# Kernel optimization log

Hardware: AMD Instinct MI355X
Metric: run time of the kernel (lower is better)

The kernel has to match this reference:

```python
import jax, jax.numpy as jnp
import numpy as np
import math

B, S, E, H = 4, 1024, 1024, 16
D = E // H
C = 1.0           # Poincare ball curvature
CS = math.sqrt(C)
EPS = 1e-7

def _sq(x):
    return jnp.sum(x * x, axis=-1, keepdims=True)

def expmap0(v):
    n = jnp.sqrt(jnp.clip(_sq(v), 1e-15))
    return jnp.tanh(CS * n) * v / (CS * n)

def logmap0(y):
    n = jnp.sqrt(jnp.clip(_sq(y), 1e-15))
    t = jnp.clip(CS * n, 0.0, 1.0 - 1e-6)
    return jnp.arctanh(t) * y / (CS * n)

def hlinear(x, z, r):
    # Poincare fully-connected layer (HNN++, Shimizu et al.), as in hypll HLinear
    lam = 2.0 / jnp.clip(1.0 - C * _sq(x), EPS)          # [..., 1] conformal factor
    zn = jnp.clip(jnp.linalg.norm(z, axis=0), 1e-15)     # [out]
    xz = x @ z                                           # [..., out]
    tcr = 2.0 * CS * r
    v = (2.0 * zn / CS) * jnp.arcsinh(CS * lam * xz / zn * jnp.cosh(tcr) - (lam - 1.0) * jnp.sinh(tcr))
    w = jnp.sinh(CS * v) / CS
    return w / (1.0 + jnp.sqrt(1.0 + C * jnp.sum(w * w, -1, keepdims=True)))

def _beta(a, b):
    return math.exp(math.lgamma(a) + math.lgamma(b) - math.lgamma(a + b))

def _forward(query, key, value, zq, bq, zk, bk, zv, bv):
    pq, pk, pv = hlinear(query, zq, bq), hlinear(key, zk, bk), hlinear(value, zv, bv)
    split = lambda x: x.reshape(B, S, H, D).transpose(0, 2, 1, 3)   # [B,H,S,D]
    q, k, v = split(pq), split(pk), split(pv)
    # attention_similarity: negative per-head pairwise Poincare distance (all heads vectorized)
    q2 = jnp.sum(q * q, -1)                              # [B,H,Sq]
    k2 = jnp.sum(k * k, -1)                              # [B,H,Sk]
    qk = jnp.einsum('bhqd,bhkd->bhqk', q, k)
    diff2 = jnp.clip(q2[..., :, None] + k2[..., None, :] - 2.0 * qk, 0.0)
    den = jnp.clip((1.0 - C * q2)[..., :, None] * (1.0 - C * k2)[..., None, :], EPS)
    dist = jnp.arccosh(jnp.clip(1.0 + 2.0 * C * diff2 / den, 1.0 + 1e-6)) / CS
    # attention_activation: softmax over keys
    w = jax.nn.softmax(-dist, axis=-1)                   # [B,H,Sq,Sk]
    # attention_midpoint: weighted gyromidpoint of values over keys
    lam = 2.0 / jnp.clip(1.0 - C * jnp.sum(v * v, -1), EPS)          # [B,H,Sk]
    num = jnp.einsum('bhqk,bhkd->bhqd', w * lam[..., None, :], v)
    dnm = jnp.clip(jnp.einsum('bhqk,bhk->bhq', jnp.abs(w), lam - 1.0), EPS)
    u = num / dnm[..., None]
    mid = u / (1.0 + jnp.sqrt(jnp.clip(1.0 - C * _sq(u), EPS)))      # (1/2) Mobius scalar mult
    # manifold.cat: beta-concatenation of heads (HNN++)
    scale = _beta(E / 2.0, 0.5) / _beta(D / 2.0, 0.5)
    tv = logmap0(mid) * scale                            # tangent at origin, [B,H,S,D]
    return expmap0(tv.transpose(0, 2, 1, 3).reshape(B, S, E))

def setup_inputs():
    key = jax.random.key(0)
    ks = jax.random.split(key, 9)
    mk = lambda k: expmap0(jax.random.normal(k, (B, S, E), jnp.float32) * (0.3 / math.sqrt(E)))
    zs = lambda k: jax.random.normal(k, (E, E), jnp.float32) / math.sqrt(E)
    bs = lambda k: jax.random.normal(k, (E,), jnp.float32) * 0.01
    return {"query": mk(ks[0]), "key": mk(ks[1]), "value": mk(ks[2]),
            "zq": zs(ks[3]), "bq": bs(ks[4]), "zk": zs(ks[5]), "bk": bs(ks[6]),
            "zv": zs(ks[7]), "bv": bs(ks[8])}

def reference(query, key, value, zq, bq, zk, bk, zv, bv):
    return _forward(query, key, value, zq, bq, zk, bk, zv, bv)
```

## Files before the change

### kernel.cpp

```cpp
#include <hip/hip_runtime.h>
#include <cmath>

#define EPSF 1e-7f

constexpr int B_ = 4, S_ = 1024, E_ = 1024, H_ = 16, D_ = 64;
constexpr int BS_ = B_ * S_;

typedef __attribute__((ext_vector_type(8))) short bf16x8;
typedef __attribute__((ext_vector_type(4))) float f32x4;

__device__ inline unsigned int fbits(float f) { union { float f; unsigned int u; } x; x.f = f; return x.u; }
__device__ inline float ubits(unsigned int u) { union { unsigned int u; float f; } x; x.u = u; return x.f; }

__device__ inline unsigned short f2bf(float f) {
  unsigned int u = fbits(f);
  unsigned int r = u + 0x7fffu + ((u >> 16) & 1u);
  return (unsigned short)(r >> 16);
}
__device__ inline float bf2f(unsigned short h) { return ubits(((unsigned int)h) << 16); }
__device__ inline float fastrcp(float x) { return __builtin_amdgcn_rcpf(x); }
__device__ inline float fastsqrt(float x) { return __builtin_amdgcn_sqrtf(x); }

__device__ __forceinline__ void async_ld16(const unsigned short* g, unsigned short* l) {
  __builtin_amdgcn_global_load_lds(
      (const __attribute__((address_space(1))) unsigned int*)g,
      (__attribute__((address_space(3))) unsigned int*)l, 16, 0, 0);
}

__device__ __forceinline__ unsigned int cvt_pk_bf16(float lo, float hi) {
  unsigned int r;
  asm("v_cvt_pk_bf16_f32 %0, %1, %2" : "=v"(r) : "v"(lo), "v"(hi));
  return r;
}
__device__ __forceinline__ void permlane32_swap(unsigned int &a, unsigned int &b) {
  asm("v_permlane32_swap_b32 %0, %1" : "+v"(a), "+v"(b));
}
__device__ __forceinline__ void permlane16_swap(unsigned int &a, unsigned int &b) {
  asm("v_permlane16_swap_b32 %0, %1" : "+v"(a), "+v"(b));
}

__global__ __launch_bounds__(256) void prep_kernel(
    const float* __restrict__ xq, const float* __restrict__ xk,
    const float* __restrict__ xv, unsigned short* __restrict__ Xbf,
    float* __restrict__ lamRow,
    const float* __restrict__ zq, const float* __restrict__ zk, const float* __restrict__ zv,
    unsigned short* __restrict__ BhiT, float* __restrict__ Zpart) {
  const int bid = blockIdx.x;
  const int tid = threadIdx.x;
  if (bid < 3 * BS_ / 4) {
    const int wid = tid >> 6, lane = tid & 63;
    const int row = bid * 4 + wid;
    const float* x = (row < BS_) ? xq : (row < 2 * BS_ ? xk : xv);
    const int r = row & (BS_ - 1);
    const float4* src = (const float4*)(x + (size_t)r * E_);
    float4 v[4];
    #pragma unroll
    for (int j = 0; j < 4; j++) v[j] = src[lane + 64 * j];
    float s = 0.f;
    #pragma unroll
    for (int j = 0; j < 4; j++)
      s += v[j].x * v[j].x + v[j].y * v[j].y + v[j].z * v[j].z + v[j].w * v[j].w;
    #pragma unroll
    for (int m = 1; m < 64; m <<= 1) s += __shfl_xor(s, m, 64);
    uint2* dst = (uint2*)(Xbf + (size_t)row * E_);
    #pragma unroll
    for (int j = 0; j < 4; j++) {
      uint2 p;
      p.x = (unsigned int)f2bf(v[j].x) | ((unsigned int)f2bf(v[j].y) << 16);
      p.y = (unsigned int)f2bf(v[j].z) | ((unsigned int)f2bf(v[j].w) << 16);
      dst[lane + 64 * j] = p;
    }
    if (lane == 0) lamRow[row] = 2.0f / fmaxf(1.0f - s, EPSF);
    return;
  }
  const int lid = bid - 3 * BS_ / 4;
  const int mat = lid >> 8;
  const int rem = lid & 255;
  const int ky = rem >> 4, nx = rem & 15;
  const float* z = mat == 0 ? zq : (mat == 1 ? zk : zv);
  const int k0 = ky * 64, n0 = nx * 64;
  __shared__ float t[64][65];
  __shared__ float sred[64][4];
  {
    int kr = tid >> 4, nc = (tid & 15) * 4;
    #pragma unroll
    for (int i = 0; i < 4; i++) {
      float4 vv = *(const float4*)(z + (size_t)(k0 + kr + i * 16) * E_ + n0 + nc);
      t[kr + i * 16][nc + 0] = vv.x;
      t[kr + i * 16][nc + 1] = vv.y;
      t[kr + i * 16][nc + 2] = vv.z;
      t[kr + i * 16][nc + 3] = vv.w;
    }
  }
  __syncthreads();
  int nr = tid >> 2, kc = (tid & 3) * 16;
  unsigned int ph[8];
  float ss = 0.f;
  #pragma unroll
  for (int p = 0; p < 8; p++) {
    float x0 = t[kc + 2 * p][nr], x1 = t[kc + 2 * p + 1][nr];
    ph[p] = (unsigned int)f2bf(x0) | ((unsigned int)f2bf(x1) << 16);
    ss += x0 * x0 + x1 * x1;
  }
  size_t off = (size_t)mat * E_ * E_ + (size_t)(n0 + nr) * E_ + k0 + kc;
  uint4* dh = (uint4*)(BhiT + off);
  dh[0] = make_uint4(ph[0], ph[1], ph[2], ph[3]);
  dh[1] = make_uint4(ph[4], ph[5], ph[6], ph[7]);
  sred[nr][tid & 3] = ss;
  __syncthreads();
  if (tid < 64) {
    float v = sred[tid][0] + sred[tid][1] + sred[tid][2] + sred[tid][3];
    Zpart[(size_t)(mat * 16 + ky) * E_ + n0 + tid] = v;
  }
}

__global__ __launch_bounds__(256, 3) void hlinear_mfma_kernel(
    const unsigned short* __restrict__ Xbf,
    const unsigned short* __restrict__ BhiT,
    const float* __restrict__ lamRow, const float* __restrict__ Zpart,
    const float* __restrict__ bq, const float* __restrict__ bk, const float* __restrict__ bv,
    unsigned short* __restrict__ Wbf) {
  const int fid = blockIdx.x;
  const int xcd = fid & 7, rest = fid >> 3;
  const int mat = rest >> 5;
  const int m0 = (rest & 31) * 128;
  const int n0 = xcd * 128;

  const unsigned short* xa = Xbf + (size_t)mat * BS_ * E_;
  const unsigned short* bh = BhiT + (size_t)mat * E_ * E_;

  __shared__ unsigned short LDSU[18432];
  __shared__ float chznS[128], shS[128], tznS[128];
  unsigned short* As = LDSU;
  unsigned short* Bh = LDSU + 8192;

  const int tid = threadIdx.x;
  const int wid = tid >> 6, lane = tid & 63, quad = lane >> 4, l16 = lane & 15;
  const int wm = (wid >> 1) * 64, wn = (wid & 1) * 64;

  if (tid < 128) {
    const int col = n0 + tid;
    float s = 0.f;
    #pragma unroll
    for (int ky = 0; ky < 16; ky++)
      s += Zpart[(size_t)(mat * 16 + ky) * E_ + col];
    float zn = fmaxf(sqrtf(s), 1e-15f);
    const float* bb = (mat == 0) ? bq : ((mat == 1) ? bk : bv);
    float rb = bb[col];
    chznS[tid] = coshf(2.f * rb) / zn;
    shS[tid] = sinhf(2.f * rb);
    tznS[tid] = 2.f * zn;
  }

  f32x4 acc[4][4];
  #pragma unroll
  for (int i = 0; i < 4; i++)
    #pragma unroll
    for (int j = 0; j < 4; j++) acc[i][j] = (f32x4){0.f, 0.f, 0.f, 0.f};

  const int lrow = lane >> 3;
  const int lcs = ((lane & 7) ^ lrow) * 8;
  const int xsw = (l16 & 7);

  for (int kt = 0; kt < E_ / 64; ++kt) {
    __syncthreads();
    const int kb = kt * 64 + lcs;
    #pragma unroll
    for (int c2 = 0; c2 < 4; c2++) {
      const int c = wid * 4 + c2;
      const int grow = c * 8 + lrow;
      async_ld16(xa + (size_t)(m0 + grow) * E_ + kb, As + c * 512);
      async_ld16(bh + (size_t)(n0 + grow) * E_ + kb, Bh + c * 512);
    }
    __syncthreads();
    #pragma unroll
    for (int h = 0; h < 2; h++) {
      bf16x8 a[4];
      #pragma unroll
      for (int mt = 0; mt < 4; mt++) {
        int row = wm + mt * 16 + l16;
        a[mt] = *(const bf16x8*)&As[row * 64 + (((h * 4 + quad) ^ xsw) * 8)];
      }
      #pragma unroll
      for (int nt = 0; nt < 4; nt++) {
        int row = wn + nt * 16 + l16;
        bf16x8 bhf = *(const bf16x8*)&Bh[row * 64 + (((h * 4 + quad) ^ xsw) * 8)];
        #pragma unroll
        for (int mt = 0; mt < 4; mt++)
          acc[mt][nt] = __builtin_amdgcn_mfma_f32_16x16x32_bf16(a[mt], bhf, acc[mt][nt], 0, 0, 0);
      }
    }
  }

  const float* lamP = lamRow + mat * BS_;
  float lamv[16];
  #pragma unroll
  for (int mt = 0; mt < 4; mt++)
    #pragma unroll
    for (int r = 0; r < 4; r++)
      lamv[mt * 4 + r] = lamP[m0 + wm + mt * 16 + quad * 4 + r];

  __syncthreads();
  unsigned short* epi = LDSU + wid * 4608;
  #pragma unroll
  for (int nt = 0; nt < 4; nt++) {
    int ci = wn + nt * 16 + l16;
    float chzn = chznS[ci];
    float sh = shS[ci];
    float tzn = tznS[ci];
    #pragma unroll
    for (int mt = 0; mt < 4; mt++) {
      #pragma unroll
      for (int r = 0; r < 4; r++) {
        float lam = lamv[mt * 4 + r];
        float arg = fmaf(lam * acc[mt][nt][r], chzn, -(lam - 1.f) * sh);
        float sq2 = sqrtf(fmaf(arg, arg, 1.f));
        float v = tzn * __logf(arg + sq2);
        float ev = __expf(v);
        float w = 0.5f * (ev - fastrcp(ev));
        epi[(mt * 16 + quad * 4 + r) * 72 + nt * 16 + l16] = f2bf(w);
      }
    }
  }
  unsigned short* gout = Wbf + (size_t)mat * BS_ * E_ + (size_t)(m0 + wm) * E_ + n0 + wn;
  const int rrow = lane >> 3, seg = lane & 7;
  #pragma unroll
  for (int i = 0; i < 8; i++) {
    int row = i * 8 + rrow;
    uint4 val = *(const uint4*)&epi[row * 72 + seg * 8];
    *(uint4*)(gout + (size_t)row * E_ + seg * 8) = val;
  }
}

__global__ __launch_bounds__(256) void normalize_kernel(
    const unsigned short* __restrict__ Wbf, unsigned short* __restrict__ Pbf,
    float* __restrict__ HN) {
  const int wid = threadIdx.x >> 6, lane = threadIdx.x & 63;
  const int row = blockIdx.x * 4 + wid;
  const unsigned short* w = Wbf + (size_t)row * E_;
  union { uint4 q[2]; unsigned short s[16]; } in;
  in.q[0] = ((const uint4*)w)[lane * 2];
  in.q[1] = ((const uint4*)w)[lane * 2 + 1];
  float wv[16];
  float s = 0.f;
  #pragma unroll
  for (int i = 0; i < 16; i++) { wv[i] = bf2f(in.s[i]); s += wv[i] * wv[i]; }
  #pragma unroll
  for (int m = 1; m < 64; m <<= 1) s += __shfl_xor(s, m, 64);
  float t = 1.f / (1.f + sqrtf(1.f + s));
  union { uint4 q[2]; unsigned short s[16]; } out;
  float hs = 0.f;
  #pragma unroll
  for (int i = 0; i < 16; i++) {
    unsigned short p = f2bf(wv[i] * t);
    out.s[i] = p;
    float r = bf2f(p);
    hs += r * r;
  }
  ((uint4*)(Pbf + (size_t)row * E_))[lane * 2] = out.q[0];
  ((uint4*)(Pbf + (size_t)row * E_))[lane * 2 + 1] = out.q[1];
  hs += __shfl_xor(hs, 1, 64);
  hs += __shfl_xor(hs, 2, 64);
  if ((lane & 3) == 0) HN[(size_t)row * H_ + (lane >> 2)] = hs;
}

__global__ __launch_bounds__(256) void vtrans_kernel(
    const unsigned short* __restrict__ Pbf, const float* __restrict__ HN,
    unsigned short* __restrict__ KsG, unsigned short* __restrict__ VtG,
    unsigned short* __restrict__ lamMG, unsigned int* __restrict__ auxG) {
  const int st = blockIdx.x, h = blockIdx.y, b = blockIdx.z;
  const unsigned short* pk = Pbf + (size_t)BS_ * E_;
  const unsigned short* pv = Pbf + (size_t)2 * BS_ * E_;
  const float* hnk = HN + (size_t)BS_ * H_;
  const float* hnv = HN + (size_t)2 * BS_ * H_;
  __shared__ unsigned short T[64][72];
  __shared__ float lamS[64], cS[64];
  const int tid = threadIdx.x;
  const size_t bhS = (size_t)(b * H_ + h) * S_;
  {
    int lr = tid >> 2, lc = (tid & 3) * 16;
    const uint4* src = (const uint4*)(pv + (size_t)(b * S_ + st * 64 + lr) * E_ + h * 64 + lc);
    *(uint4*)&T[lr][lc] = src[0];
    *(uint4*)&T[lr][lc + 8] = src[1];
  }
  if (tid < 64) {
    float v2 = hnv[(size_t)(b * S_ + st * 64 + tid) * H_ + h];
    float lam = 2.f / fmaxf(1.f - v2, EPSF);
    lamS[tid] = lam;
    size_t sidx = bhS + st * 64 + tid;
    lamMG[sidx] = f2bf(lam - 1.f);
    float k2 = hnk[(size_t)(b * S_ + st * 64 + tid) * H_ + h];
    float rc = fastrcp(1.f - k2);
    cS[tid] = rc;
    auxG[sidx] = (unsigned int)f2bf(rc) | ((unsigned int)f2bf(rc * k2) << 16);
  }
  __syncthreads();
  {
    int d = tid >> 2, sc = (tid & 3) * 16;
    unsigned int o[8];
    #pragma unroll
    for (int i = 0; i < 8; i++) {
      int s0 = sc + 2 * i;
      float f0 = bf2f(T[s0][d]) * lamS[s0];
      float f1 = bf2f(T[s0 + 1][d]) * lamS[s0 + 1];
      o[i] = (unsigned int)f2bf(f0) | ((unsigned int)f2bf(f1) << 16);
    }
    unsigned short* dst = VtG + (bhS * 64) + (size_t)d * S_ + st * 64 + sc;
    ((uint4*)dst)[0] = make_uint4(o[0], o[1], o[2], o[3]);
    ((uint4*)dst)[1] = make_uint4(o[4], o[5], o[6], o[7]);
  }
  {
    int lr = tid >> 2, lc = (tid & 3) * 16;
    float c = cS[lr];
    const uint4* src = (const uint4*)(pk + (size_t)(b * S_ + st * 64 + lr) * E_ + h * 64 + lc);
    union { uint4 q; unsigned short s[8]; } i0, i1, o0, o1;
    i0.q = src[0]; i1.q = src[1];
    #pragma unroll
    for (int j = 0; j < 8; j++) {
      o0.s[j] = f2bf(bf2f(i0.s[j]) * c);
      o1.s[j] = f2bf(bf2f(i1.s[j]) * c);
    }
    unsigned short* dst = KsG + (bhS + st * 64 + lr) * 64 + lc;
    ((uint4*)dst)[0] = o0.q;
    ((uint4*)dst)[1] = o1.q;
  }
}

__global__ __launch_bounds__(512) void attention_kernel(
    const unsigned short* __restrict__ Pbf, const float* __restrict__ HN,
    const unsigned short* __restrict__ KsG, const unsigned short* __restrict__ VtG,
    const unsigned short* __restrict__ lamMG, const unsigned int* __restrict__ auxG,
    float* __restrict__ TV, float scale) {
  const int fid = blockIdx.x;
  const int xcd = fid & 7, slot = fid >> 3;
  const int group = xcd + 8 * (slot >> 3);
  const int qt = slot & 7;
  const int h = group & 15, b = group >> 4;

  const unsigned short* pq = Pbf;
  const float* hnq = HN;

  const int tid = threadIdx.x;
  const int wid = tid >> 6, lane = tid & 63;
  const int quad = lane >> 4, l16 = lane & 15;

  __shared__ __align__(16) unsigned short Kl[2][8192];
  __shared__ __align__(16) unsigned short Vl[2][8192];
  __shared__ __align__(16) unsigned short lamL[1024];
  __shared__ __align__(16) unsigned int auxL[1024];

  const size_t bhS = (size_t)(b * H_ + h) * S_;
  const int lr = lane >> 3, cch = lane & 7;
  const int xsw = l16 & 7;
  const unsigned short* kbase = KsG + bhS * 64;
  const unsigned short* vbase = VtG + bhS * 64;
  const int srow = wid * 8 + lr;
  const int scc = ((cch ^ lr) * 8);

  async_ld16(kbase + (size_t)srow * 64 + scc, &Kl[0][wid * 512]);
  async_ld16(kbase + (size_t)(64 + srow) * 64 + scc, &Kl[0][4096 + wid * 512]);
  async_ld16(vbase + (size_t)srow * S_ + scc, &Vl[0][wid * 512]);
  async_ld16(vbase + (size_t)srow * S_ + 64 + scc, &Vl[0][4096 + wid * 512]);

  ((unsigned int*)lamL)[tid] = ((const unsigned int*)(lamMG + bhS))[tid];
  ((uint2*)auxL)[tid] = ((const uint2*)(auxG + bhS))[tid];

  const int qrow0 = qt * 128 + wid * 16;
  const size_t qgrow = ((size_t)(b * S_ + qrow0 + l16)) * E_ + h * 64;
  bf16x8 aq0r = *(const bf16x8*)(pq + qgrow + quad * 8);
  bf16x8 aq1r = *(const bf16x8*)(pq + qgrow + 32 + quad * 8);
  const float q2l = hnq[((size_t)(b * S_ + qrow0 + l16)) * H_ + h];
  const float al = 2.f * fastrcp(1.f - q2l);
  const float sc2 = -2.f * al;
  bf16x8 aq0, aq1;
  #pragma unroll
  for (int j = 0; j < 8; j++) {
    aq0[j] = (short)f2bf(bf2f((unsigned short)aq0r[j]) * sc2);
    aq1[j] = (short)f2bf(bf2f((unsigned short)aq1r[j]) * sc2);
  }
  const unsigned short ae0 = (quad == 0) ? f2bf(al * q2l) : 0;
  const unsigned short ae1 = (quad == 0) ? f2bf(al) : 0;
  const bf16x8 aex = (bf16x8){(short)ae0, (short)ae1, 0, 0, 0, 0, 0, 0};

  f32x4 accO[4];
  #pragma unroll
  for (int dt = 0; dt < 4; dt++) accO[dt] = (f32x4){0.f, 0.f, 0.f, 0.f};
  f32x4 accD = (f32x4){0.f, 0.f, 0.f, 0.f};

  asm volatile("s_waitcnt vmcnt(0) lgkmcnt(0)" ::: "memory");
  __builtin_amdgcn_s_barrier();

  const int NIT = S_ / 128;
  int buf = 0;
  #pragma unroll 1
  for (int it = 0; it < NIT; ++it) {
    if (it + 1 < NIT) {
      const int kr0 = (it + 1) * 128;
      async_ld16(kbase + (size_t)(kr0 + srow) * 64 + scc, &Kl[buf ^ 1][wid * 512]);
      async_ld16(kbase + (size_t)(kr0 + 64 + srow) * 64 + scc, &Kl[buf ^ 1][4096 + wid * 512]);
      async_ld16(vbase + (size_t)srow * S_ + kr0 + scc, &Vl[buf ^ 1][wid * 512]);
      async_ld16(vbase + (size_t)srow * S_ + kr0 + 64 + scc, &Vl[buf ^ 1][4096 + wid * 512]);
    }
    #pragma unroll
    for (int half = 0; half < 2; half++) {
      const int kt = it * 2 + half;
      const unsigned short* Kb = &Kl[buf][half * 4096];
      const unsigned short* Vb = &Vl[buf][half * 4096];

      unsigned int Wp[4][2];
      #pragma unroll
      for (int nt = 0; nt < 4; nt++) {
        const int krow = nt * 16 + l16;
        bf16x8 bk0 = *(const bf16x8*)&Kb[krow * 64 + ((quad ^ xsw) * 8)];
        bf16x8 bk1 = *(const bf16x8*)&Kb[krow * 64 + (((4 + quad) ^ xsw) * 8)];
        unsigned int av = (quad == 0) ? auxL[kt * 64 + krow] : 0u;
        bf16x8 bex = (bf16x8){(short)(av & 0xFFFF), (short)(av >> 16), 0, 0, 0, 0, 0, 0};
        f32x4 z = (f32x4){0.f, 0.f, 0.f, 0.f};
        f32x4 st = __builtin_amdgcn_mfma_f32_16x16x32_bf16(bex, aex, z, 0, 0, 0);
        st = __builtin_amdgcn_mfma_f32_16x16x32_bf16(bk0, aq0, st, 0, 0, 0);
        st = __builtin_amdgcn_mfma_f32_16x16x32_bf16(bk1, aq1, st, 0, 0, 0);
        float w[4];
        #pragma unroll
        for (int r2 = 0; r2 < 4; r2++) {
          float t = fmaxf(st[r2], 1e-6f);
          float A = 1.f + t;
          w[r2] = A - fastsqrt(fmaf(A, A, -1.f));
        }
        Wp[nt][0] = cvt_pk_bf16(w[0], w[1]);
        Wp[nt][1] = cvt_pk_bf16(w[2], w[3]);
      }
      unsigned int x00 = Wp[0][0], y00 = Wp[1][0];
      permlane32_swap(x00, y00); permlane16_swap(x00, y00);
      unsigned int x01 = Wp[0][1], y01 = Wp[1][1];
      permlane32_swap(x01, y01); permlane16_swap(x01, y01);
      unsigned int x10 = Wp[2][0], y10 = Wp[3][0];
      permlane32_swap(x10, y10); permlane16_swap(x10, y10);
      unsigned int x11 = Wp[2][1], y11 = Wp[3][1];
      permlane32_swap(x11, y11); permlane16_swap(x11, y11);
      union { unsigned int u[4]; bf16x8 v; } ap0u, ap1u;
      ap0u.u[0] = x00; ap0u.u[1] = x01; ap0u.u[2] = y00; ap0u.u[3] = y01;
      ap1u.u[0] = x10; ap1u.u[1] = x11; ap1u.u[2] = y10; ap1u.u[3] = y11;
      const bf16x8 ap0 = ap0u.v, ap1 = ap1u.v;

      #pragma unroll
      for (int dt = 0; dt < 4; dt++) {
        const int drow = dt * 16 + l16;
        bf16x8 bv0 = *(const bf16x8*)&Vb[drow * 64 + ((quad ^ xsw) * 8)];
        bf16x8 bv1 = *(const bf16x8*)&Vb[drow * 64 + (((4 + quad) ^ xsw) * 8)];
        accO[dt] = __builtin_amdgcn_mfma_f32_16x16x32_bf16(ap0, bv0, accO[dt], 0, 0, 0);
        accO[dt] = __builtin_amdgcn_mfma_f32_16x16x32_bf16(ap1, bv1, accO[dt], 0, 0, 0);
      }
      bf16x8 bl0 = *(const bf16x8*)&lamL[kt * 64 + quad * 8];
      bf16x8 bl1 = *(const bf16x8*)&lamL[kt * 64 + 32 + quad * 8];
      accD = __builtin_amdgcn_mfma_f32_16x16x32_bf16(ap0, bl0, accD, 0, 0, 0);
      accD = __builtin_amdgcn_mfma_f32_16x16x32_bf16(ap1, bl1, accD, 0, 0, 0);
    }

    asm volatile("s_waitcnt vmcnt(0)" ::: "memory");
    __builtin_amdgcn_s_barrier();
    buf ^= 1;
  }

  #pragma unroll
  for (int r2 = 0; r2 < 4; r2++) {
    float rdsum = fastrcp(accD[r2]);
    float uu[4];
    float su = 0.f;
    #pragma unroll
    for (int dt = 0; dt < 4; dt++) { uu[dt] = accO[dt][r2] * rdsum; su += uu[dt] * uu[dt]; }
    su += __shfl_xor(su, 1, 64);
    su += __shfl_xor(su, 2, 64);
    su += __shfl_xor(su, 4, 64);
    su += __shfl_xor(su, 8, 64);
    float g = fastrcp(1.f + fastsqrt(fmaxf(1.f - su, EPSF)));
    float n2 = fmaxf(su * g * g, 1e-15f);
    float n = fastsqrt(n2);
    float fac = atanhf(fminf(n, 1.f - 1e-6f)) * fastrcp(n) * g * scale;
    size_t orow = ((size_t)(b * S_ + qrow0 + quad * 4 + r2)) * E_ + h * 64 + l16;
    #pragma unroll
    for (int dt = 0; dt < 4; dt++) TV[orow + dt * 16] = fac * uu[dt];
  }
}

__global__ __launch_bounds__(256) void expmap_kernel(float* __restrict__ TV) {
  const int wid = threadIdx.x >> 6, lane = threadIdx.x & 63;
  const int row = blockIdx.x * 4 + wid;
  float* w = TV + (size_t)row * E_;
  float4 v[4];
  #pragma unroll
  for (int j = 0; j < 4; j++) v[j] = ((float4*)w)[lane + 64 * j];
  float s = 0.f;
  #pragma unroll
  for (int j = 0; j < 4; j++)
    s += v[j].x * v[j].x + v[j].y * v[j].y + v[j].z * v[j].z + v[j].w * v[j].w;
  #pragma unroll
  for (int m = 1; m < 64; m <<= 1) s += __shfl_xor(s, m, 64);
  float n = sqrtf(fmaxf(s, 1e-15f));
  float f = tanhf(n) / n;
  #pragma unroll
  for (int j = 0; j < 4; j++) {
    v[j].x *= f; v[j].y *= f; v[j].z *= f; v[j].w *= f;
    ((float4*)w)[lane + 64 * j] = v[j];
  }
}

extern "C" void kernel_launch(void* const* d_in, const int* in_sizes, int n_in,
                              void* d_out, int out_size, void* d_ws, size_t ws_size,
                              hipStream_t stream) {
  (void)in_sizes; (void)n_in; (void)out_size; (void)ws_size;
  const float* q  = (const float*)d_in[0];
  const float* k  = (const float*)d_in[1];
  const float* v  = (const float*)d_in[2];
  const float* zq = (const float*)d_in[3];
  const float* bq = (const float*)d_in[4];
  const float* zk = (const float*)d_in[5];
  const float* bk = (const float*)d_in[6];
  const float* zv = (const float*)d_in[7];
  const float* bv = (const float*)d_in[8];

  unsigned short* Wbf = (unsigned short*)d_ws;
  unsigned short* Pbf = Wbf + (size_t)3 * BS_ * E_;
  unsigned short* BhiT = Pbf;
  unsigned short* Xbf = Pbf + (size_t)3 * BS_ * E_;
  float* HN           = (float*)(Xbf + (size_t)3 * BS_ * E_);
  float* lamRow       = HN + (size_t)3 * BS_ * H_;
  float* Zpart        = lamRow + 3 * BS_;
  unsigned short* VtG = (unsigned short*)(Zpart + 48 * E_);
  unsigned short* KsG = VtG + (size_t)B_ * H_ * 64 * S_;
  unsigned short* lamMG = KsG + (size_t)B_ * H_ * S_ * 64;
  unsigned int* auxG  = (unsigned int*)(lamMG + (size_t)B_ * H_ * S_);
  float* out          = (float*)d_out;

  double lb1 = lgamma(E_ / 2.0) + lgamma(0.5) - lgamma(E_ / 2.0 + 0.5);
  double lb2 = lgamma(D_ / 2.0) + lgamma(0.5) - lgamma(D_ / 2.0 + 0.5);
  float scale = (float)exp(lb1 - lb2);

  hipLaunchKernelGGL(prep_kernel, dim3(3 * BS_ / 4 + 768), dim3(256), 0, stream,
                     q, k, v, Xbf, lamRow, zq, zk, zv, BhiT, Zpart);
  hipLaunchKernelGGL(hlinear_mfma_kernel, dim3(768), dim3(256), 0, stream,
                     Xbf, BhiT, lamRow, Zpart, bq, bk, bv, Wbf);
  hipLaunchKernelGGL(normalize_kernel, dim3(3 * BS_ / 4), dim3(256), 0, stream, Wbf, Pbf, HN);
  hipLaunchKernelGGL(vtrans_kernel, dim3(16, 16, 4), dim3(256), 0, stream,
                     Pbf, HN, KsG, VtG, lamMG, auxG);
  hipLaunchKernelGGL(attention_kernel, dim3(512), dim3(512), 0, stream,
                     Pbf, HN, KsG, VtG, lamMG, auxG, out, scale);
  hipLaunchKernelGGL(expmap_kernel, dim3(BS_ / 4), dim3(256), 0, stream, out);
}
```

Baseline: 219.8 us.

## Fuse K scaling and V lambda into normalize; remap hlinear blocks per XCD

The normalize kernel now computes the per-head K scaling (1/(1-|k|^2)), aux values and V conformal-factor scaling directly from its registers. It writes K straight into the head-major KsG layout and V pre-scaled into Pbf. This leaves vtrans as a pure transpose and removes one read of K, the HN round-trip for k/v, and the extra float math in vtrans. Separately, the hlinear block-to-tile mapping is changed so each XCD handles a contiguous set of M tiles across all N tiles, aiming for better L2 reuse of the X rows. Writes from normalize to KsG are scattered per head (64-element chunks), which may be less coalesced.

```diff
diff --git a/kernel.cpp b/kernel.cpp
--- a/kernel.cpp
+++ b/kernel.cpp
@@ -121,10 +121,11 @@
     const float* __restrict__ bq, const float* __restrict__ bk, const float* __restrict__ bv,
     unsigned short* __restrict__ Wbf) {
   const int fid = blockIdx.x;
-  const int xcd = fid & 7, rest = fid >> 3;
-  const int mat = rest >> 5;
-  const int m0 = (rest & 31) * 128;
-  const int n0 = xcd * 128;
+  const int xcd = fid & 7, j = fid >> 3;
+  const int n0 = (j & 7) * 128;
+  const int gp = xcd * 12 + (j >> 3);
+  const int mat = gp >> 5;
+  const int m0 = (gp & 31) * 128;
 
   const unsigned short* xa = Xbf + (size_t)mat * BS_ * E_;
   const unsigned short* bh = BhiT + (size_t)mat * E_ * E_;
@@ -156,7 +157,7 @@
   #pragma unroll
   for (int i = 0; i < 4; i++)
     #pragma unroll
-    for (int j = 0; j < 4; j++) acc[i][j] = (f32x4){0.f, 0.f, 0.f, 0.f};
+    for (int jj = 0; jj < 4; jj++) acc[i][jj] = (f32x4){0.f, 0.f, 0.f, 0.f};
 
   const int lrow = lane >> 3;
   const int lcs = ((lane & 7) ^ lrow) * 8;
@@ -234,7 +235,9 @@
 
 __global__ __launch_bounds__(256) void normalize_kernel(
     const unsigned short* __restrict__ Wbf, unsigned short* __restrict__ Pbf,
-    float* __restrict__ HN) {
+    float* __restrict__ HN,
+    unsigned short* __restrict__ KsG, unsigned short* __restrict__ lamMG,
+    unsigned int* __restrict__ auxG) {
   const int wid = threadIdx.x >> 6, lane = threadIdx.x & 63;
   const int row = blockIdx.x * 4 + wid;
   const unsigned short* w = Wbf + (size_t)row * E_;
@@ -249,81 +252,70 @@
   for (int m = 1; m < 64; m <<= 1) s += __shfl_xor(s, m, 64);
   float t = 1.f / (1.f + sqrtf(1.f + s));
   union { uint4 q[2]; unsigned short s[16]; } out;
+  float rv[16];
   float hs = 0.f;
   #pragma unroll
   for (int i = 0; i < 16; i++) {
     unsigned short p = f2bf(wv[i] * t);
     out.s[i] = p;
-    float r = bf2f(p);
-    hs += r * r;
-  }
-  ((uint4*)(Pbf + (size_t)row * E_))[lane * 2] = out.q[0];
-  ((uint4*)(Pbf + (size_t)row * E_))[lane * 2 + 1] = out.q[1];
+    rv[i] = bf2f(p);
+    hs += rv[i] * rv[i];
+  }
   hs += __shfl_xor(hs, 1, 64);
   hs += __shfl_xor(hs, 2, 64);
-  if ((lane & 3) == 0) HN[(size_t)row * H_ + (lane >> 2)] = hs;
+  const int mat = row >= 2 * BS_ ? 2 : (row >= BS_ ? 1 : 0);
+  const int r4 = row & (BS_ - 1);
+  const int b = r4 >> 10, key = r4 & (S_ - 1);
+  const int head = lane >> 2;
+  const size_t bhS = ((size_t)(b * H_ + head)) * S_;
+  if (mat == 0) {
+    ((uint4*)(Pbf + (size_t)row * E_))[lane * 2] = out.q[0];
+    ((uint4*)(Pbf + (size_t)row * E_))[lane * 2 + 1] = out.q[1];
+    if ((lane & 3) == 0) HN[(size_t)r4 * H_ + head] = hs;
+  } else if (mat == 1) {
+    float c = fastrcp(1.f - hs);
+    union { uint4 q[2]; unsigned short s[16]; } ks;
+    #pragma unroll
+    for (int i = 0; i < 16; i++) ks.s[i] = f2bf(rv[i] * c);
+    unsigned short* dst = KsG + (bhS + key) * 64 + (lane & 3) * 16;
+    ((uint4*)dst)[0] = ks.q[0];
+    ((uint4*)dst)[1] = ks.q[1];
+    if ((lane & 3) == 0)
+      auxG[bhS + key] = (unsigned int)f2bf(c) | ((unsigned int)f2bf(c * hs) << 16);
+  } else {
+    float lam = 2.f / fmaxf(1.f - hs, EPSF);
+    union { uint4 q[2]; unsigned short s[16]; } pv;
+    #pragma unroll
+    for (int i = 0; i < 16; i++) pv.s[i] = f2bf(rv[i] * lam);
+    ((uint4*)(Pbf + (size_t)row * E_))[lane * 2] = pv.q[0];
+    ((uint4*)(Pbf + (size_t)row * E_))[lane * 2 + 1] = pv.q[1];
+    if ((lane & 3) == 0) lamMG[bhS + key] = f2bf(lam - 1.f);
+  }
 }
 
 __global__ __launch_bounds__(256) void vtrans_kernel(
-    const unsigned short* __restrict__ Pbf, const float* __restrict__ HN,
-    unsigned short* __restrict__ KsG, unsigned short* __restrict__ VtG,
-    unsigned short* __restrict__ lamMG, unsigned int* __restrict__ auxG) {
+    const unsigned short* __restrict__ PvF, unsigned short* __restrict__ VtG) {
   const int st = blockIdx.x, h = blockIdx.y, b = blockIdx.z;
-  const unsigned short* pk = Pbf + (size_t)BS_ * E_;
-  const unsigned short* pv = Pbf + (size_t)2 * BS_ * E_;
-  const float* hnk = HN + (size_t)BS_ * H_;
-  const float* hnv = HN + (size_t)2 * BS_ * H_;
   __shared__ unsigned short T[64][72];
-  __shared__ float lamS[64], cS[64];
   const int tid = threadIdx.x;
   const size_t bhS = (size_t)(b * H_ + h) * S_;
   {
     int lr = tid >> 2, lc = (tid & 3) * 16;
-    const uint4* src = (const uint4*)(pv + (size_t)(b * S_ + st * 64 + lr) * E_ + h * 64 + lc);
+    const uint4* src = (const uint4*)(PvF + (size_t)(b * S_ + st * 64 + lr) * E_ + h * 64 + lc);
     *(uint4*)&T[lr][lc] = src[0];
     *(uint4*)&T[lr][lc + 8] = src[1];
   }
-  if (tid < 64) {
-    float v2 = hnv[(size_t)(b * S_ + st * 64 + tid) * H_ + h];
-    float lam = 2.f / fmaxf(1.f - v2, EPSF);
-    lamS[tid] = lam;
-    size_t sidx = bhS + st * 64 + tid;
-    lamMG[sidx] = f2bf(lam - 1.f);
-    float k2 = hnk[(size_t)(b * S_ + st * 64 + tid) * H_ + h];
-    float rc = fastrcp(1.f - k2);
-    cS[tid] = rc;
-    auxG[sidx] = (unsigned int)f2bf(rc) | ((unsigned int)f2bf(rc * k2) << 16);
-  }
   __syncthreads();
-  {
-    int d = tid >> 2, sc = (tid & 3) * 16;
-    unsigned int o[8];
-    #pragma unroll
-    for (int i = 0; i < 8; i++) {
-      int s0 = sc + 2 * i;
-      float f0 = bf2f(T[s0][d]) * lamS[s0];
-      float f1 = bf2f(T[s0 + 1][d]) * lamS[s0 + 1];
-      o[i] = (unsigned int)f2bf(f0) | ((unsigned int)f2bf(f1) << 16);
-    }
-    unsigned short* dst = VtG + (bhS * 64) + (size_t)d * S_ + st * 64 + sc;
-    ((uint4*)dst)[0] = make_uint4(o[0], o[1], o[2], o[3]);
-    ((uint4*)dst)[1] = make_uint4(o[4], o[5], o[6], o[7]);
-  }
-  {
-    int lr = tid >> 2, lc = (tid & 3) * 16;
-    float c = cS[lr];
-    const uint4* src = (const uint4*)(pk + (size_t)(b * S_ + st * 64 + lr) * E_ + h * 64 + lc);
-    union { uint4 q; unsigned short s[8]; } i0, i1, o0, o1;
-    i0.q = src[0]; i1.q = src[1];
-    #pragma unroll
-    for (int j = 0; j < 8; j++) {
-      o0.s[j] = f2bf(bf2f(i0.s[j]) * c);
-      o1.s[j] = f2bf(bf2f(i1.s[j]) * c);
-    }
-    unsigned short* dst = KsG + (bhS + st * 64 + lr) * 64 + lc;
-    ((uint4*)dst)[0] = o0.q;
-    ((uint4*)dst)[1] = o1.q;
-  }
+  int d = tid >> 2, sc = (tid & 3) * 16;
+  unsigned int o[8];
+  #pragma unroll
+  for (int i = 0; i < 8; i++) {
+    int s0 = sc + 2 * i;
+    o[i] = (unsigned int)T[s0][d] | ((unsigned int)T[s0 + 1][d] << 16);
+  }
+  unsigned short* dst = VtG + bhS * 64 + (size_t)d * S_ + st * 64 + sc;
+  ((uint4*)dst)[0] = make_uint4(o[0], o[1], o[2], o[3]);
+  ((uint4*)dst)[1] = make_uint4(o[4], o[5], o[6], o[7]);
 }
 
 __global__ __launch_bounds__(512) void attention_kernel(
@@ -529,6 +521,7 @@
   unsigned short* KsG = VtG + (size_t)B_ * H_ * 64 * S_;
   unsigned short* lamMG = KsG + (size_t)B_ * H_ * S_ * 64;
   unsigned int* auxG  = (unsigned int*)(lamMG + (size_t)B_ * H_ * S_);
+  unsigned short* PvF = Pbf + (size_t)2 * BS_ * E_;
   float* out          = (float*)d_out;
 
   double lb1 = lgamma(E_ / 2.0) + lgamma(0.5) - lgamma(E_ / 2.0 + 0.5);
@@ -539,9 +532,9 @@
                      q, k, v, Xbf, lamRow, zq, zk, zv, BhiT, Zpart);
   hipLaunchKernelGGL(hlinear_mfma_kernel, dim3(768), dim3(256), 0, stream,
                      Xbf, BhiT, lamRow, Zpart, bq, bk, bv, Wbf);
-  hipLaunchKernelGGL(normalize_kernel, dim3(3 * BS_ / 4), dim3(256), 0, stream, Wbf, Pbf, HN);
-  hipLaunchKernelGGL(vtrans_kernel, dim3(16, 16, 4), dim3(256), 0, stream,
-                     Pbf, HN, KsG, VtG, lamMG, auxG);
+  hipLaunchKernelGGL(normalize_kernel, dim3(3 * BS_ / 4), dim3(256), 0, stream,
+                     Wbf, Pbf, HN, KsG, lamMG, auxG);
+  hipLaunchKernelGGL(vtrans_kernel, dim3(16, 16, 4), dim3(256), 0, stream, PvF, VtG);
   hipLaunchKernelGGL(attention_kernel, dim3(512), dim3(512), 0, stream,
                      Pbf, HN, KsG, VtG, lamMG, auxG, out, scale);
   hipLaunchKernelGGL(expmap_kernel, dim3(BS_ / 4), dim3(256), 0, stream, out);
```

Result: faster. 214.9 us (-2.2%).
